# Kernel optimization log

Measured on AMD Instinct MI355X. Metric: run time of the kernel, lower is better.

Reference implementation:

```python
import jax, jax.numpy as jnp
import numpy as np

S, B, D_IN, D_OUT, E, R = 2048, 8, 1024, 4096, 8, 16

def setup_inputs() -> dict:
    key = jax.random.key(0)
    ks = jax.random.split(key, 6)
    x = jax.random.normal(ks[0], (S, B, D_IN), dtype=jnp.float32)
    gate_w = jax.random.normal(ks[1], (E, D_IN), dtype=jnp.float32) * 0.01  # std=0.01 init
    gate_b = jnp.zeros((E,), dtype=jnp.float32)  # init_lambda = 0
    W = jax.random.normal(ks[2], (D_OUT, D_IN), dtype=jnp.float32) * 0.02
    bias = jax.random.normal(ks[3], (D_OUT,), dtype=jnp.float32) * 0.02
    lora_A = jax.random.normal(ks[4], (E, R, D_IN), dtype=jnp.float32) * 0.02
    lora_B = jax.random.normal(ks[5], (E, D_OUT, R), dtype=jnp.float32) * 0.02
    return {"x": x, "gate_w": gate_w, "gate_b": gate_b, "W": W, "bias": bias,
            "lora_A": lora_A, "lora_B": lora_B}

def reference(x, gate_w, gate_b, W, bias, lora_A, lora_B):
    # gate: Linear(hidden, E) applied tokenwise, then mean over seq dim (dim 0, batch_first=False)
    gates = jnp.einsum('sbd,ed->sbe', x, gate_w) + gate_b      # [S,B,E]
    gate_weights = gates.mean(axis=0)                           # [B,E]
    # per-expert LoRA delta (detached in the torch original)
    delta = jnp.einsum('eor,eri->eoi', lora_B, lora_A)          # [E,D_OUT,D_IN]
    delta = jax.lax.stop_gradient(delta)
    # per-sample merged weight: W + sum_e g[b,e] * delta[e]
    W_b = W[None] + jnp.einsum('be,eoi->boi', gate_weights, delta)  # [B,D_OUT,D_IN]
    # per-sample linear (equivalent to looping functional_call over samples)
    out = jnp.einsum('sbi,boi->sbo', x, W_b) + bias             # [S,B,D_OUT]
    return out
```

## Files before the change

### kernel.cpp

```cpp
#include <hip/hip_runtime.h>
#include <stdint.h>

typedef unsigned short u16;
typedef __bf16 bf16x8 __attribute__((ext_vector_type(8)));
typedef float  f32x4  __attribute__((ext_vector_type(4)));

#define SDIM 2048
#define BDIM 8
#define DIN  1024
#define DOUT 4096
#define EDIM 8
#define RDIM 16
#define KAUG 1152
#define MDIM (SDIM*BDIM)
#define SCH  32
#define NT2  18

__device__ __forceinline__ u16 f2bf(float f) {
    __bf16 h = (__bf16)f;
    return __builtin_bit_cast(u16, h);
}

__device__ __forceinline__ void gload16(const u16* g, u16* lds) {
    __builtin_amdgcn_global_load_lds(
        (const __attribute__((address_space(1))) void*)g,
        (__attribute__((address_space(3))) void*)lds, 16, 0, 0);
}

#define VMCNT(n)  asm volatile("s_waitcnt vmcnt(" #n ")" ::: "memory")
#define BARF()    do { asm volatile("" ::: "memory");                \
                       __builtin_amdgcn_s_barrier();                 \
                       asm volatile("" ::: "memory"); } while (0)

__global__ __launch_bounds__(256) void k1_reduce_convert(
    const float* __restrict__ x, u16* __restrict__ Xb, float* __restrict__ P)
{
    const int b  = blockIdx.x;
    const int sc = blockIdx.y;
    const int i  = threadIdx.x * 4;
    float a0 = 0.f, a1 = 0.f, a2 = 0.f, a3 = 0.f;
    const int s0 = sc * (SDIM / SCH);
    for (int s = s0; s < s0 + (SDIM / SCH); ++s) {
        const float4 v = *reinterpret_cast<const float4*>(
            &x[((size_t)s * BDIM + b) * DIN + i]);
        a0 += v.x; a1 += v.y; a2 += v.z; a3 += v.w;
        ushort4 u{f2bf(v.x), f2bf(v.y), f2bf(v.z), f2bf(v.w)};
        *reinterpret_cast<ushort4*>(&Xb[((size_t)s * BDIM + b) * KAUG + i]) = u;
    }
    float4 p{a0, a1, a2, a3};
    *reinterpret_cast<float4*>(&P[((size_t)sc * BDIM + b) * DIN + i]) = p;
}

__global__ __launch_bounds__(256) void k2_gates(
    const float* __restrict__ P, const float* __restrict__ gw,
    const float* __restrict__ gb, float* __restrict__ g)
{
    const int e = blockIdx.x, b = blockIdx.y, t = threadIdx.x;
    float dot = 0.f;
    for (int i = t; i < DIN; i += 256) {
        float xs = 0.f;
        #pragma unroll
        for (int c = 0; c < SCH; ++c) xs += P[((size_t)c * BDIM + b) * DIN + i];
        dot += xs * gw[(size_t)e * DIN + i];
    }
    __shared__ float red[256];
    red[t] = dot;
    __syncthreads();
    #pragma unroll
    for (int off = 128; off > 0; off >>= 1) {
        if (t < off) red[t] += red[t + off];
        __syncthreads();
    }
    if (t == 0) g[b * EDIM + e] = red[0] * (1.0f / SDIM) + gb[e];
}

__global__ __launch_bounds__(256) void kw_build_waug(
    const float* __restrict__ W, const float* __restrict__ lb, u16* __restrict__ Waug)
{
    const int o = blockIdx.x, t = threadIdx.x;
    for (int i = t; i < DIN; i += 256)
        Waug[(size_t)o * KAUG + i] = f2bf(W[(size_t)o * DIN + i]);
    if (t < EDIM * RDIM) {
        const int e = t >> 4, r = t & 15;
        Waug[(size_t)o * KAUG + DIN + t] =
            f2bf(lb[((size_t)e * DOUT + o) * RDIM + r]);
    }
}

__global__ __launch_bounds__(256) void kl_convert(
    const float* __restrict__ la, u16* __restrict__ LAb)
{
    const int idx = blockIdx.x * 256 + threadIdx.x;
    if (idx < EDIM * RDIM * DIN) LAb[idx] = f2bf(la[idx]);
}

__global__ __launch_bounds__(256) void k4_scale_u(
    const float* __restrict__ T, const float* __restrict__ g, u16* __restrict__ Xb)
{
    const int idx = blockIdx.x * 256 + threadIdx.x;
    const int m = idx >> 7, er = idx & 127;
    const int b = m & (BDIM - 1), e = er >> 4;
    const float u = g[b * EDIM + e] * T[idx];
    Xb[(size_t)m * KAUG + DIN + er] = f2bf(u);
}

template <int ADD_BIAS>
__global__ __launch_bounds__(256) void gemm_bt(
    const u16* __restrict__ A, int lda,
    const u16* __restrict__ B, int ldb,
    float* __restrict__ C, int ldc,
    const float* __restrict__ bias, int ktiles)
{
    __shared__ __align__(16) u16 As[128][64];
    __shared__ __align__(16) u16 Bs[128][64];

    const int tid  = threadIdx.x;
    const int lane = tid & 63;
    const int l15  = lane & 15;
    const int l4   = lane >> 4;
    const int sw   = lane & 7;
    const int wid  = tid >> 6;
    const int wr   = wid >> 1;
    const int wc   = wid & 1;
    const int m0 = blockIdx.y * 128;
    const int n0 = blockIdx.x * 128;

    f32x4 acc[4][4] = {};

    for (int kt = 0; kt < ktiles; ++kt) {
        #pragma unroll
        for (int ii = 0; ii < 4; ++ii) {
            const int cix = ii * 256 + tid;
            const int row = cix >> 3, cl = cix & 7;
            const int kof = kt * 64 + ((cl ^ (row & 7)) << 3);
            gload16(A + (size_t)(m0 + row) * lda + kof, &As[0][0] + cix * 8);
            gload16(B + (size_t)(n0 + row) * ldb + kof, &Bs[0][0] + cix * 8);
        }
        __syncthreads();
        #pragma unroll
        for (int ks = 0; ks < 2; ++ks) {
            bf16x8 av[4], bv[4];
            #pragma unroll
            for (int mi = 0; mi < 4; ++mi)
                av[mi] = *reinterpret_cast<const bf16x8*>(
                    &As[wr * 64 + mi * 16 + l15][((ks * 4 + l4) ^ sw) << 3]);
            #pragma unroll
            for (int ni = 0; ni < 4; ++ni)
                bv[ni] = *reinterpret_cast<const bf16x8*>(
                    &Bs[wc * 64 + ni * 16 + l15][((ks * 4 + l4) ^ sw) << 3]);
            #pragma unroll
            for (int mi = 0; mi < 4; ++mi)
                #pragma unroll
                for (int ni = 0; ni < 4; ++ni)
                    acc[mi][ni] = __builtin_amdgcn_mfma_f32_16x16x32_bf16(
                        av[mi], bv[ni], acc[mi][ni], 0, 0, 0);
        }
        __syncthreads();
    }

    #pragma unroll
    for (int mi = 0; mi < 4; ++mi) {
        const int r0 = m0 + wr * 64 + mi * 16 + l4 * 4;
        #pragma unroll
        for (int ni = 0; ni < 4; ++ni) {
            const int col = n0 + wc * 64 + ni * 16 + l15;
            const float badd = ADD_BIAS ? bias[col] : 0.0f;
            float* cp = C + (size_t)r0 * ldc + col;
            #pragma unroll
            for (int r = 0; r < 4; ++r)
                cp[(size_t)r * ldc] = acc[mi][ni][r] + badd;
        }
    }
}

__global__ __launch_bounds__(512) void gemm_main(
    const u16* __restrict__ A, const u16* __restrict__ Bm,
    float* __restrict__ C, const float* __restrict__ bias)
{
    __shared__ __align__(16) u16 As[2][2][128][64];
    __shared__ __align__(16) u16 Bs[2][2][128][64];

    const int tid  = threadIdx.x;
    const int lane = tid & 63;
    const int l15  = lane & 15;
    const int l4   = lane >> 4;
    const int sw   = lane & 7;
    const int wid  = tid >> 6;
    const int wm   = wid >> 2;
    const int wn   = wid & 3;
    const int bh   = wn >> 1;
    const int bl   = wn & 1;

    const int f   = blockIdx.x + blockIdx.y * gridDim.x;
    const int cpx = (gridDim.x * gridDim.y) >> 3;
    const int s_  = (f & 7) * cpx + (f >> 3);
    const int m0  = (s_ / gridDim.x) * 256;
    const int n0  = (s_ % gridDim.x) * 256;

    f32x4  acc[8][4] = {};
    bf16x8 aq[2][2], bv[4][2];

    auto stage = [&](int s) {
        const int t = s >> 2, part = s & 3, buf = t & 1, hf = part & 1;
        #pragma unroll
        for (int ii = 0; ii < 2; ++ii) {
            const int cix = ii * 512 + tid;
            const int row = cix >> 3, cl = cix & 7;
            const int kof = t * 64 + ((cl ^ (row & 7)) << 3);
            if (part < 2)
                gload16(A + (size_t)(m0 + hf * 128 + row) * KAUG + kof,
                        &As[buf][hf][0][0] + cix * 8);
            else
                gload16(Bm + (size_t)(n0 + hf * 128 + row) * KAUG + kof,
                        &Bs[buf][hf][0][0] + cix * 8);
        }
    };

    stage(0); stage(1); stage(2); stage(3); stage(4);
    VMCNT(2);
    BARF();

    #define PHASE(P)                                                            \
    do {                                                                        \
        if ((P) == 0) {                                                         \
            _Pragma("unroll") for (int nf = 0; nf < 4; ++nf)                    \
                _Pragma("unroll") for (int kk = 0; kk < 2; ++kk)                \
                    bv[nf][kk] = *reinterpret_cast<const bf16x8*>(              \
                        &Bs[buf][bh][bl * 64 + nf * 16 + l15]                   \
                           [((kk * 4 + l4) ^ sw) << 3]);                        \
        }                                                                       \
        _Pragma("unroll") for (int fr = 0; fr < 2; ++fr)                        \
            _Pragma("unroll") for (int kk = 0; kk < 2; ++kk)                    \
                aq[fr][kk] = *reinterpret_cast<const bf16x8*>(                  \
                    &As[buf][wm][(P) * 32 + fr * 16 + l15]                      \
                       [((kk * 4 + l4) ^ sw) << 3]);                            \
        { const int su = 4 * j + 5 + (P); if (su < 4 * NT2) stage(su); }        \
        __builtin_amdgcn_s_setprio(1);                                          \
        _Pragma("unroll") for (int kk = 0; kk < 2; ++kk)                        \
            _Pragma("unroll") for (int fr = 0; fr < 2; ++fr)                    \
                _Pragma("unroll") for (int nf = 0; nf < 4; ++nf)                \
                    acc[(P) * 2 + fr][nf] =                                     \
                        __builtin_amdgcn_mfma_f32_16x16x32_bf16(                \
                            aq[fr][kk], bv[nf][kk], acc[(P) * 2 + fr][nf],      \
                            0, 0, 0);                                           \
        __builtin_amdgcn_s_setprio(0);                                          \
        if ((P) == 3) { if (j < NT2 - 2) VMCNT(2); else VMCNT(0); }             \
        BARF();                                                                 \
    } while (0)

    for (int j = 0; j < NT2; ++j) {
        const int buf = j & 1;
        PHASE(0);
        PHASE(1);
        PHASE(2);
        PHASE(3);
    }
    #undef PHASE

    #pragma unroll
    for (int a = 0; a < 8; ++a) {
        const int row0 = m0 + wm * 128 + a * 16 + l4 * 4;
        #pragma unroll
        for (int nf = 0; nf < 4; ++nf) {
            const int col = n0 + wn * 64 + nf * 16 + l15;
            const float badd = bias[col];
            float* cp = C + (size_t)row0 * DOUT + col;
            #pragma unroll
            for (int q = 0; q < 4; ++q)
                cp[(size_t)q * DOUT] = acc[a][nf][q] + badd;
        }
    }
}

extern "C" void kernel_launch(void* const* d_in, const int* in_sizes, int n_in,
                              void* d_out, int out_size, void* d_ws, size_t ws_size,
                              hipStream_t stream)
{
    const float* x    = (const float*)d_in[0];
    const float* gw   = (const float*)d_in[1];
    const float* gb   = (const float*)d_in[2];
    const float* W    = (const float*)d_in[3];
    const float* bias = (const float*)d_in[4];
    const float* la   = (const float*)d_in[5];
    const float* lb   = (const float*)d_in[6];
    float* out = (float*)d_out;

    char* ws = (char*)d_ws;
    u16*   Xb   = (u16*)(ws);
    u16*   Waug = (u16*)(ws + 37748736);
    float* T    = (float*)(ws + 47185920);
    float* P    = (float*)(ws + 55574528);
    u16*   LAb  = (u16*)(ws + 56623104);
    float* G    = (float*)(ws + 56885248);

    k1_reduce_convert<<<dim3(BDIM, SCH), 256, 0, stream>>>(x, Xb, P);
    kw_build_waug<<<DOUT, 256, 0, stream>>>(W, lb, Waug);
    kl_convert<<<(EDIM * RDIM * DIN + 255) / 256, 256, 0, stream>>>(la, LAb);
    k2_gates<<<dim3(EDIM, BDIM), 256, 0, stream>>>(P, gw, gb, G);
    gemm_bt<0><<<dim3(1, MDIM / 128), 256, 0, stream>>>(
        Xb, KAUG, LAb, DIN, T, EDIM * RDIM, nullptr, DIN / 64);
    k4_scale_u<<<(MDIM * EDIM * RDIM) / 256, 256, 0, stream>>>(T, G, Xb);
    gemm_main<<<dim3(DOUT / 256, MDIM / 256), 512, 0, stream>>>(
        Xb, Waug, out, bias);
}
```

Before: 239.8 us.

## Fuse gate scaling into LoRA GEMM epilogue and remap main GEMM tile order per XCD

```diff
diff --git a/kernel.cpp b/kernel.cpp
--- a/kernel.cpp
+++ b/kernel.cpp
@@ -94,22 +94,9 @@
     if (idx < EDIM * RDIM * DIN) LAb[idx] = f2bf(la[idx]);
 }
 
-__global__ __launch_bounds__(256) void k4_scale_u(
-    const float* __restrict__ T, const float* __restrict__ g, u16* __restrict__ Xb)
-{
-    const int idx = blockIdx.x * 256 + threadIdx.x;
-    const int m = idx >> 7, er = idx & 127;
-    const int b = m & (BDIM - 1), e = er >> 4;
-    const float u = g[b * EDIM + e] * T[idx];
-    Xb[(size_t)m * KAUG + DIN + er] = f2bf(u);
-}
-
-template <int ADD_BIAS>
-__global__ __launch_bounds__(256) void gemm_bt(
-    const u16* __restrict__ A, int lda,
-    const u16* __restrict__ B, int ldb,
-    float* __restrict__ C, int ldc,
-    const float* __restrict__ bias, int ktiles)
+__global__ __launch_bounds__(256) void gemm_lora(
+    const u16* __restrict__ A, const u16* __restrict__ B,
+    const float* __restrict__ G, u16* __restrict__ Xb)
 {
     __shared__ __align__(16) u16 As[128][64];
     __shared__ __align__(16) u16 Bs[128][64];
@@ -123,18 +110,17 @@
     const int wr   = wid >> 1;
     const int wc   = wid & 1;
     const int m0 = blockIdx.y * 128;
-    const int n0 = blockIdx.x * 128;
 
     f32x4 acc[4][4] = {};
 
-    for (int kt = 0; kt < ktiles; ++kt) {
+    for (int kt = 0; kt < DIN / 64; ++kt) {
         #pragma unroll
         for (int ii = 0; ii < 4; ++ii) {
             const int cix = ii * 256 + tid;
             const int row = cix >> 3, cl = cix & 7;
             const int kof = kt * 64 + ((cl ^ (row & 7)) << 3);
-            gload16(A + (size_t)(m0 + row) * lda + kof, &As[0][0] + cix * 8);
-            gload16(B + (size_t)(n0 + row) * ldb + kof, &Bs[0][0] + cix * 8);
+            gload16(A + (size_t)(m0 + row) * KAUG + kof, &As[0][0] + cix * 8);
+            gload16(B + (size_t)row * DIN + kof, &Bs[0][0] + cix * 8);
         }
         __syncthreads();
         #pragma unroll
@@ -163,12 +149,14 @@
         const int r0 = m0 + wr * 64 + mi * 16 + l4 * 4;
         #pragma unroll
         for (int ni = 0; ni < 4; ++ni) {
-            const int col = n0 + wc * 64 + ni * 16 + l15;
-            const float badd = ADD_BIAS ? bias[col] : 0.0f;
-            float* cp = C + (size_t)r0 * ldc + col;
-            #pragma unroll
-            for (int r = 0; r < 4; ++r)
-                cp[(size_t)r * ldc] = acc[mi][ni][r] + badd;
+            const int col = wc * 64 + ni * 16 + l15;
+            const int e   = col >> 4;
+            #pragma unroll
+            for (int r = 0; r < 4; ++r) {
+                const int row = r0 + r;
+                const float gv = G[((row & 7) << 3) + e];
+                Xb[(size_t)row * KAUG + DIN + col] = f2bf(gv * acc[mi][ni][r]);
+            }
         }
     }
 }
@@ -192,10 +180,10 @@
     const int bl   = wn & 1;
 
     const int f   = blockIdx.x + blockIdx.y * gridDim.x;
-    const int cpx = (gridDim.x * gridDim.y) >> 3;
-    const int s_  = (f & 7) * cpx + (f >> 3);
-    const int m0  = (s_ / gridDim.x) * 256;
-    const int n0  = (s_ % gridDim.x) * 256;
+    const int xcd = f & 7, k = f >> 3;
+    const int gn  = xcd & 3, gm = xcd >> 2;
+    const int n0  = (gn * 4 + (k & 3)) * 256;
+    const int m0  = (gm * 32 + (k >> 2)) * 256;
 
     f32x4  acc[8][4] = {};
     bf16x8 aq[2][2], bv[4][2];
@@ -288,18 +276,15 @@
     char* ws = (char*)d_ws;
     u16*   Xb   = (u16*)(ws);
     u16*   Waug = (u16*)(ws + 37748736);
-    float* T    = (float*)(ws + 47185920);
-    float* P    = (float*)(ws + 55574528);
-    u16*   LAb  = (u16*)(ws + 56623104);
-    float* G    = (float*)(ws + 56885248);
+    float* P    = (float*)(ws + 47185920);
+    u16*   LAb  = (u16*)(ws + 48234496);
+    float* G    = (float*)(ws + 48496640);
 
     k1_reduce_convert<<<dim3(BDIM, SCH), 256, 0, stream>>>(x, Xb, P);
     kw_build_waug<<<DOUT, 256, 0, stream>>>(W, lb, Waug);
     kl_convert<<<(EDIM * RDIM * DIN + 255) / 256, 256, 0, stream>>>(la, LAb);
     k2_gates<<<dim3(EDIM, BDIM), 256, 0, stream>>>(P, gw, gb, G);
-    gemm_bt<0><<<dim3(1, MDIM / 128), 256, 0, stream>>>(
-        Xb, KAUG, LAb, DIN, T, EDIM * RDIM, nullptr, DIN / 64);
-    k4_scale_u<<<(MDIM * EDIM * RDIM) / 256, 256, 0, stream>>>(T, G, Xb);
+    gemm_lora<<<dim3(1, MDIM / 128), 256, 0, stream>>>(Xb, LAb, G, Xb);
     gemm_main<<<dim3(DOUT / 256, MDIM / 256), 512, 0, stream>>>(
         Xb, Waug, out, bias);
 }
```

Result: no change. 238.9 us (-0.4%).
